# Kernel tuning notes

Hardware: AMD Instinct MI355X
Metric: run time of the kernel (lower is better)

Reference implementation:

```python
import jax, jax.numpy as jnp
import numpy as np

BATCH = 1024
A = 128  # image height
B = 128  # image width (must equal A for the original matmul chain to type-check)
N = 64   # attention grid size
H = 1024 # h_dim


def setup_inputs() -> dict:
    key = jax.random.key(0)
    k0, k1, k2, k3 = jax.random.split(key, 4)
    x = jax.random.normal(k0, (BATCH, A * B), dtype=jnp.float32)
    x_hat = jax.random.normal(k1, (BATCH, A * B), dtype=jnp.float32)
    h = jax.random.normal(k2, (BATCH, H), dtype=jnp.float32)
    W_read_w = jax.random.normal(k3, (5, H), dtype=jnp.float32) * 0.02
    W_read_b = jnp.zeros((5,), dtype=jnp.float32)
    return {"x": x, "x_hat": x_hat, "h": h, "W_read_w": W_read_w, "W_read_b": W_read_b}


def _compute_filterbanks(params):
    # params: (5,) from W_read(h)[0]
    gt_X, gt_Y, log_var, log_dt = params[0], params[1], params[2], params[3]
    var = jnp.exp(log_var + 1e-8)
    # .item() in the original detaches these from the autograd graph
    g_X = jax.lax.stop_gradient((A + 1) * (gt_X + 1) / 2)
    g_Y = jax.lax.stop_gradient((B + 1) * (gt_Y + 1) / 2)
    d = jax.lax.stop_gradient(jnp.exp(log_dt) * (max(A, B) - 1) / (N - 1))
    # linspace(g + (-N/2-0.5)d, g + (N-1-N/2-0.5)d, N) == g + (i - N/2 - 0.5)*d
    idx = jnp.arange(N, dtype=jnp.float32) - N / 2 - 0.5  # (N,)
    mu_X = g_X + idx * d  # (N,)
    mu_Y = g_Y + idx * d  # (N,)
    a = jnp.arange(A, dtype=jnp.float32)
    b = jnp.arange(B, dtype=jnp.float32)
    F_X = jnp.exp(-((a[None, :] - mu_X[:, None]) ** 2) / (2 * var))  # (N, A)
    F_Y = jnp.exp(-((b[None, :] - mu_Y[:, None]) ** 2) / (2 * var))  # (N, B)
    # NOTE: original normalizes by the GLOBAL sum, not per-row
    F_X = F_X / jnp.sum(F_X)
    F_Y = F_Y / jnp.sum(F_Y)
    return F_X, F_Y


def reference(x, x_hat, h, W_read_w, W_read_b):
    # params from FIRST batch element, shared across the whole batch (as in original)
    params = (h @ W_read_w.T + W_read_b)[0]  # (5,)
    gamma = jnp.exp(params[4])
    F_X, F_Y = _compute_filterbanks(params)  # (N,A), (N,B)

    xi = x.reshape(-1, A, B)
    xh = x_hat.reshape(-1, A, B)

    def filt(z):  # gamma * F_Y @ z @ F_X.T  -> (batch, N, N)
        t = jnp.einsum('na,kab->knb', F_Y, z)      # (batch, N, B)
        return gamma * jnp.einsum('knb,mb->knm', t, F_X)

    x_filt = filt(xi).reshape(-1, N * N)
    x_hat_filt = filt(xh).reshape(-1, N * N)
    return jnp.concatenate([x_filt, x_hat_filt], axis=1)  # (batch, 2*N*N)
```

## Files before the change

### kernel.cpp

```cpp
#include <hip/hip_runtime.h>
#include <math.h>

#define AB 128
#define NN 64
#define HD 1024

#define SFZ 256.0f
#define SFF 64.0f
#define DESCALE (1.0f / 1048576.0f)

typedef _Float16 half8 __attribute__((ext_vector_type(8)));
typedef float f32x4 __attribute__((ext_vector_type(4)));
typedef unsigned u32x4 __attribute__((ext_vector_type(4)));


__device__ __forceinline__ float wave_reduce(float v) {
  v += __shfl_down(v, 32);
  v += __shfl_down(v, 16);
  v += __shfl_down(v, 8);
  v += __shfl_down(v, 4);
  v += __shfl_down(v, 2);
  v += __shfl_down(v, 1);
  return v;
}

__global__ __launch_bounds__(1024) void fb_setup(
    const float* __restrict__ h, const float* __restrict__ Ww,
    const float* __restrict__ Wb, void* __restrict__ wsv) {
  __shared__ float redp[16][5];
  __shared__ float reds[16][2];
  __shared__ float sc[5];
  __shared__ float ssum[2];
  const int tid = threadIdx.x;
  const int lane = tid & 63;
  const int wv = tid >> 6;

  const float hv = h[tid];
  float p[5];
#pragma unroll
  for (int j = 0; j < 5; ++j) p[j] = hv * Ww[j * HD + tid];
#pragma unroll
  for (int j = 0; j < 5; ++j) {
    float r = wave_reduce(p[j]);
    if (lane == 0) redp[wv][j] = r;
  }
  __syncthreads();
  if (tid < 5) {
    float s = Wb[tid];
#pragma unroll
    for (int w = 0; w < 16; ++w) s += redp[w][tid];
    sc[tid] = s;
  }
  __syncthreads();

  const float gt_X = sc[0], gt_Y = sc[1], log_var = sc[2], log_dt = sc[3];
  const float var = expf(log_var + 1e-8f);
  const float g_X = (129.0f * (gt_X + 1.0f)) / 2.0f;
  const float g_Y = (129.0f * (gt_Y + 1.0f)) / 2.0f;
  const float d = (expf(log_dt) * 127.0f) / 63.0f;
  const float twovar = 2.0f * var;

  float fyv[8], fxv[8];
  float sY = 0.f, sX = 0.f;
#pragma unroll
  for (int c = 0; c < 8; ++c) {
    const int idx = tid + 1024 * c;
    const int n = idx >> 7;
    const int col = idx & 127;
    const float idxn = (float)n - 32.5f;
    const float muX = g_X + idxn * d;
    const float muY = g_Y + idxn * d;
    const float dx = (float)col - muX;
    const float dy = (float)col - muY;
    const float fx = expf(-(dx * dx) / twovar);
    const float fy = expf(-(dy * dy) / twovar);
    fyv[c] = fy;
    fxv[c] = fx;
    sY += fy;
    sX += fx;
  }
  {
    float rY = wave_reduce(sY);
    float rX = wave_reduce(sX);
    if (lane == 0) { reds[wv][0] = rY; reds[wv][1] = rX; }
  }
  __syncthreads();
  if (tid < 2) {
    float s = 0.f;
#pragma unroll
    for (int w = 0; w < 16; ++w) s += reds[w][tid];
    ssum[tid] = s;
  }
  __syncthreads();
  const float invY = 1.0f / ssum[0];
  const float invX = 1.0f / ssum[1];

  _Float16* FXk = (_Float16*)wsv;
  _Float16* FYhi = (_Float16*)wsv + 2 * NN * AB;
  _Float16* FYlo = FYhi + NN * AB;

#pragma unroll
  for (int c = 0; c < 8; ++c) {
    const int idx = tid + 1024 * c;
    const int n = idx >> 7;
    const int col = idx & 127;
    const float vy = fyv[c] * invY * SFF;
    const float vx = fxv[c] * invX * SFF;
    const _Float16 yh = (_Float16)vy;
    const _Float16 xh2 = (_Float16)vx;
    FYhi[idx] = yh;
    FYlo[idx] = (_Float16)(vy - (float)yh);
    const int kaddr = ((col >> 3) << 9) + (n << 3) + (col & 7);
    FXk[kaddr] = xh2;
    FXk[8192 + kaddr] = (_Float16)(vx - (float)xh2);
  }
  if (tid == 0) ((float*)wsv)[16384] = expf(sc[4]) * DESCALE;
}

__device__ __forceinline__ void split8(const f32x4 z0, const f32x4 z1,
                                       float s, half8& hi, half8& lo) {
#pragma unroll
  for (int e = 0; e < 8; ++e) {
    const float q = (e < 4 ? z0[e] : z1[e - 4]) * s;
    const _Float16 hh = (_Float16)q;
    hi[e] = hh;
    lo[e] = (_Float16)(q - (float)hh);
  }
}

#define ZLD(dst, base, OFF)                                              \
  asm volatile("global_load_dwordx4 %0, %1, off offset:" #OFF            \
               : "=v"(dst) : "v"(base))

#define WAITVM_SB(N)                                                     \
  do {                                                                   \
    asm volatile("s_waitcnt vmcnt(" #N ")");                             \
    __builtin_amdgcn_sched_barrier(0);                                   \
  } while (0)

__global__ __launch_bounds__(256, 4) void fb_filt(
    const float* __restrict__ x, const float* __restrict__ xh,
    const void* __restrict__ wsv, float* __restrict__ out) {
  __shared__ __align__(16) _Float16 S_lds[2 * NN * AB];

  const int tid = threadIdx.x;
  const int lane = tid & 63;
  const int wv = tid >> 6;
  const int l15 = lane & 15;
  const int h4 = lane >> 4;
  const int bid = blockIdx.x;
  const int img = bid >> 1;
  const int which = bid & 1;
  const float* __restrict__ Z = (which ? xh : x) + (size_t)img * (AB * AB);
  const _Float16* __restrict__ FYhi = (const _Float16*)wsv + 2 * NN * AB;
  const _Float16* __restrict__ FYlo = FYhi + NN * AB;
  const float gamma_eff = ((const float*)wsv)[16384];

  {
    const u32x4* __restrict__ src = (const u32x4*)wsv;
    u32x4* __restrict__ dst = (u32x4*)S_lds;
#pragma unroll
    for (int c = 0; c < 8; ++c) dst[c * 256 + tid] = src[c * 256 + tid];
  }
  __syncthreads();

  const float* zb0 = Z + (32 * wv + l15) * AB + 8 * h4;
  const float* zb1 = zb0 + 16 * AB;
  f32x4 z0_0, z0_1, z0_2, z0_3, z1_0, z1_1, z1_2, z1_3;
  f32x4 z2_0, z2_1, z2_2, z2_3, z3_0, z3_1, z3_2, z3_3;
  ZLD(z0_0, zb0, 0);   ZLD(z0_1, zb0, 16);
  ZLD(z0_2, zb1, 0);   ZLD(z0_3, zb1, 16);
  ZLD(z1_0, zb0, 128); ZLD(z1_1, zb0, 144);
  ZLD(z1_2, zb1, 128); ZLD(z1_3, zb1, 144);
  ZLD(z2_0, zb0, 256); ZLD(z2_1, zb0, 272);
  ZLD(z2_2, zb1, 256); ZLD(z2_3, zb1, 272);
  ZLD(z3_0, zb0, 384); ZLD(z3_1, zb0, 400);
  ZLD(z3_2, zb1, 384); ZLD(z3_3, zb1, 400);

  f32x4 acc[4][2];
#pragma unroll
  for (int mt = 0; mt < 4; ++mt)
#pragma unroll
    for (int j = 0; j < 2; ++j) acc[mt][j] = {0.f, 0.f, 0.f, 0.f};

#define S1_KS(KS, WN)                                                          \
  do {                                                                         \
    WAITVM_SB(WN);                                                             \
    half8 bhi0, blo0, bhi1, blo1;                                              \
    split8(z##KS##_0, z##KS##_1, SFZ, bhi0, blo0);                             \
    split8(z##KS##_2, z##KS##_3, SFZ, bhi1, blo1);                             \
    const int gbase = ((4 * (KS) + h4) << 9);                                  \
    _Pragma("unroll")                                                          \
    for (int mt = 0; mt < 4; ++mt) {                                           \
      const _Float16* ap = S_lds + gbase + ((16 * mt + l15) << 3);             \
      const half8 ahi = *(const half8*)ap;                                     \
      const half8 alo = *(const half8*)(ap + 8192);                            \
      acc[mt][0] = __builtin_amdgcn_mfma_f32_16x16x32_f16(ahi, bhi0, acc[mt][0], 0, 0, 0); \
      acc[mt][0] = __builtin_amdgcn_mfma_f32_16x16x32_f16(ahi, blo0, acc[mt][0], 0, 0, 0); \
      acc[mt][0] = __builtin_amdgcn_mfma_f32_16x16x32_f16(alo, bhi0, acc[mt][0], 0, 0, 0); \
      acc[mt][1] = __builtin_amdgcn_mfma_f32_16x16x32_f16(ahi, bhi1, acc[mt][1], 0, 0, 0); \
      acc[mt][1] = __builtin_amdgcn_mfma_f32_16x16x32_f16(ahi, blo1, acc[mt][1], 0, 0, 0); \
      acc[mt][1] = __builtin_amdgcn_mfma_f32_16x16x32_f16(alo, bhi1, acc[mt][1], 0, 0, 0); \
    }                                                                          \
  } while (0)

  S1_KS(0, 12);
  S1_KS(1, 8);
  S1_KS(2, 4);
  S1_KS(3, 0);
#undef S1_KS

  __syncthreads();

  half8 fyh[4], fyl[4];
#pragma unroll
  for (int ks = 0; ks < 4; ++ks) {
    const int foff = (16 * wv + l15) * AB + 32 * ks + 8 * h4;
    fyh[ks] = *(const half8*)(FYhi + foff);
    fyl[ks] = *(const half8*)(FYlo + foff);
  }

#pragma unroll
  for (int mt = 0; mt < 4; ++mt) {
#pragma unroll
    for (int j = 0; j < 2; ++j) {
      const int abase = ((4 * wv + 2 * j + (l15 >> 3)) << 9) + (l15 & 7);
#pragma unroll
      for (int r = 0; r < 4; ++r) {
        const int row = 16 * mt + 4 * h4 + r;
        const float v = acc[mt][j][r];
        const _Float16 hh = (_Float16)v;
        const _Float16 ll = (_Float16)(v - (float)hh);
        S_lds[abase + (row << 3)] = hh;
        S_lds[8192 + abase + (row << 3)] = ll;
      }
    }
  }
  __syncthreads();

  f32x4 acc2[4];
#pragma unroll
  for (int mt = 0; mt < 4; ++mt) acc2[mt] = {0.f, 0.f, 0.f, 0.f};

#pragma unroll
  for (int ks = 0; ks < 4; ++ks) {
    const int gbase = ((4 * ks + h4) << 9);
#pragma unroll
    for (int mt = 0; mt < 4; ++mt) {
      const _Float16* bp = S_lds + gbase + ((16 * mt + l15) << 3);
      const half8 bh = *(const half8*)bp;
      const half8 bl = *(const half8*)(bp + 8192);
      acc2[mt] = __builtin_amdgcn_mfma_f32_16x16x32_f16(fyh[ks], bh, acc2[mt], 0, 0, 0);
      acc2[mt] = __builtin_amdgcn_mfma_f32_16x16x32_f16(fyh[ks], bl, acc2[mt], 0, 0, 0);
      acc2[mt] = __builtin_amdgcn_mfma_f32_16x16x32_f16(fyl[ks], bh, acc2[mt], 0, 0, 0);
    }
  }

  float* __restrict__ ob = out + (size_t)img * 8192 + which * 4096;
#pragma unroll
  for (int mt = 0; mt < 4; ++mt) {
#pragma unroll
    for (int r = 0; r < 4; ++r) {
      ob[(16 * wv + 4 * h4 + r) * 64 + 16 * mt + l15] = acc2[mt][r] * gamma_eff;
    }
  }
}

extern "C" void kernel_launch(void* const* d_in, const int* in_sizes, int n_in,
                              void* d_out, int out_size, void* d_ws, size_t ws_size,
                              hipStream_t stream) {
  const float* x = (const float*)d_in[0];
  const float* xh = (const float*)d_in[1];
  const float* h = (const float*)d_in[2];
  const float* Ww = (const float*)d_in[3];
  const float* Wb = (const float*)d_in[4];
  float* outp = (float*)d_out;

  fb_setup<<<1, 1024, 0, stream>>>(h, Ww, Wb, d_ws);
  fb_filt<<<2048, 256, 0, stream>>>(x, xh, (const void*)d_ws, outp);
}
```

Measured before the change: 178.8 us.

## Assign one image per wave with per-wave LDS staging and pipelined chunk loads

Each wave now processes a whole 128x128 image in four 32-row chunks instead of four waves cooperating on one image. Stage-1 results go to a private LDS region per wave, so the inter-stage __syncthreads barriers disappear. The next chunk's Z and F_Y loads are issued ahead of stage 2 to overlap global memory with MFMA work. F_Y is stored in a K-blocked layout to suit the new loads. The grid shrinks to 512 blocks and occupancy is lowered to 2 blocks per CU because of the larger LDS footprint and register use, which may reduce latency hiding.

Measured after the change: 181.7 us. No clear change (+1.6%).

```diff
diff --git a/kernel.cpp b/kernel.cpp
--- a/kernel.cpp
+++ b/kernel.cpp
@@ -12,6 +12,8 @@
 typedef _Float16 half8 __attribute__((ext_vector_type(8)));
 typedef float f32x4 __attribute__((ext_vector_type(4)));
 typedef unsigned u32x4 __attribute__((ext_vector_type(4)));
+
+#define MFMA16 __builtin_amdgcn_mfma_f32_16x16x32_f16
 
 
 __device__ __forceinline__ float wave_reduce(float v) {
@@ -96,8 +98,7 @@
   const float invX = 1.0f / ssum[1];
 
   _Float16* FXk = (_Float16*)wsv;
-  _Float16* FYhi = (_Float16*)wsv + 2 * NN * AB;
-  _Float16* FYlo = FYhi + NN * AB;
+  _Float16* FYk = (_Float16*)wsv + 2 * NN * AB;
 
 #pragma unroll
   for (int c = 0; c < 8; ++c) {
@@ -108,11 +109,11 @@
     const float vx = fxv[c] * invX * SFF;
     const _Float16 yh = (_Float16)vy;
     const _Float16 xh2 = (_Float16)vx;
-    FYhi[idx] = yh;
-    FYlo[idx] = (_Float16)(vy - (float)yh);
     const int kaddr = ((col >> 3) << 9) + (n << 3) + (col & 7);
     FXk[kaddr] = xh2;
     FXk[8192 + kaddr] = (_Float16)(vx - (float)xh2);
+    FYk[kaddr] = yh;
+    FYk[8192 + kaddr] = (_Float16)(vy - (float)yh);
   }
   if (tid == 0) ((float*)wsv)[16384] = expf(sc[4]) * DESCALE;
 }
@@ -138,23 +139,23 @@
     __builtin_amdgcn_sched_barrier(0);                                   \
   } while (0)
 
-__global__ __launch_bounds__(256, 4) void fb_filt(
+__global__ __launch_bounds__(256, 2) void fb_filt(
     const float* __restrict__ x, const float* __restrict__ xh,
     const void* __restrict__ wsv, float* __restrict__ out) {
-  __shared__ __align__(16) _Float16 S_lds[2 * NN * AB];
+  __shared__ __align__(16) _Float16 S_lds[32768];
 
   const int tid = threadIdx.x;
   const int lane = tid & 63;
   const int wv = tid >> 6;
   const int l15 = lane & 15;
   const int h4 = lane >> 4;
-  const int bid = blockIdx.x;
-  const int img = bid >> 1;
-  const int which = bid & 1;
+  const int slot = (blockIdx.x << 2) | wv;
+  const int img = slot >> 1;
+  const int which = slot & 1;
   const float* __restrict__ Z = (which ? xh : x) + (size_t)img * (AB * AB);
-  const _Float16* __restrict__ FYhi = (const _Float16*)wsv + 2 * NN * AB;
-  const _Float16* __restrict__ FYlo = FYhi + NN * AB;
+  const _Float16* __restrict__ FYk = (const _Float16*)wsv + 2 * NN * AB;
   const float gamma_eff = ((const float*)wsv)[16384];
+  const int Tb = 16384 + (wv << 12);
 
   {
     const u32x4* __restrict__ src = (const u32x4*)wsv;
@@ -164,104 +165,149 @@
   }
   __syncthreads();
 
-  const float* zb0 = Z + (32 * wv + l15) * AB + 8 * h4;
-  const float* zb1 = zb0 + 16 * AB;
   f32x4 z0_0, z0_1, z0_2, z0_3, z1_0, z1_1, z1_2, z1_3;
   f32x4 z2_0, z2_1, z2_2, z2_3, z3_0, z3_1, z3_2, z3_3;
-  ZLD(z0_0, zb0, 0);   ZLD(z0_1, zb0, 16);
-  ZLD(z0_2, zb1, 0);   ZLD(z0_3, zb1, 16);
-  ZLD(z1_0, zb0, 128); ZLD(z1_1, zb0, 144);
-  ZLD(z1_2, zb1, 128); ZLD(z1_3, zb1, 144);
-  ZLD(z2_0, zb0, 256); ZLD(z2_1, zb0, 272);
-  ZLD(z2_2, zb1, 256); ZLD(z2_3, zb1, 272);
-  ZLD(z3_0, zb0, 384); ZLD(z3_1, zb0, 400);
-  ZLD(z3_2, zb1, 384); ZLD(z3_3, zb1, 400);
-
+  half8 fyh[4], fyl[4];
   f32x4 acc[4][2];
-#pragma unroll
-  for (int mt = 0; mt < 4; ++mt)
-#pragma unroll
-    for (int j = 0; j < 2; ++j) acc[mt][j] = {0.f, 0.f, 0.f, 0.f};
-
-#define S1_KS(KS, WN)                                                          \
-  do {                                                                         \
-    WAITVM_SB(WN);                                                             \
-    half8 bhi0, blo0, bhi1, blo1;                                              \
-    split8(z##KS##_0, z##KS##_1, SFZ, bhi0, blo0);                             \
-    split8(z##KS##_2, z##KS##_3, SFZ, bhi1, blo1);                             \
-    const int gbase = ((4 * (KS) + h4) << 9);                                  \
-    _Pragma("unroll")                                                          \
-    for (int mt = 0; mt < 4; ++mt) {                                           \
-      const _Float16* ap = S_lds + gbase + ((16 * mt + l15) << 3);             \
-      const half8 ahi = *(const half8*)ap;                                     \
-      const half8 alo = *(const half8*)(ap + 8192);                            \
-      acc[mt][0] = __builtin_amdgcn_mfma_f32_16x16x32_f16(ahi, bhi0, acc[mt][0], 0, 0, 0); \
-      acc[mt][0] = __builtin_amdgcn_mfma_f32_16x16x32_f16(ahi, blo0, acc[mt][0], 0, 0, 0); \
-      acc[mt][0] = __builtin_amdgcn_mfma_f32_16x16x32_f16(alo, bhi0, acc[mt][0], 0, 0, 0); \
-      acc[mt][1] = __builtin_amdgcn_mfma_f32_16x16x32_f16(ahi, bhi1, acc[mt][1], 0, 0, 0); \
-      acc[mt][1] = __builtin_amdgcn_mfma_f32_16x16x32_f16(ahi, blo1, acc[mt][1], 0, 0, 0); \
-      acc[mt][1] = __builtin_amdgcn_mfma_f32_16x16x32_f16(alo, bhi1, acc[mt][1], 0, 0, 0); \
-    }                                                                          \
-  } while (0)
-
-  S1_KS(0, 12);
-  S1_KS(1, 8);
-  S1_KS(2, 4);
-  S1_KS(3, 0);
-#undef S1_KS
-
-  __syncthreads();
-
-  half8 fyh[4], fyl[4];
-#pragma unroll
-  for (int ks = 0; ks < 4; ++ks) {
-    const int foff = (16 * wv + l15) * AB + 32 * ks + 8 * h4;
-    fyh[ks] = *(const half8*)(FYhi + foff);
-    fyl[ks] = *(const half8*)(FYlo + foff);
-  }
-
-#pragma unroll
-  for (int mt = 0; mt < 4; ++mt) {
-#pragma unroll
-    for (int j = 0; j < 2; ++j) {
-      const int abase = ((4 * wv + 2 * j + (l15 >> 3)) << 9) + (l15 & 7);
+  f32x4 acc2[4][4];
+#pragma unroll
+  for (int nt = 0; nt < 4; ++nt)
+#pragma unroll
+    for (int mt = 0; mt < 4; ++mt) acc2[nt][mt] = {0.f, 0.f, 0.f, 0.f};
+
+#define ISSUE_Z(AC)                                                      \
+  do {                                                                   \
+    const float* zc0_ = Z + (32 * (AC) + l15) * AB + 8 * h4;             \
+    const float* zc1_ = zc0_ + 16 * AB;                                  \
+    ZLD(z0_0, zc0_, 0);   ZLD(z0_1, zc0_, 16);                           \
+    ZLD(z0_2, zc1_, 0);   ZLD(z0_3, zc1_, 16);                           \
+    ZLD(z1_0, zc0_, 128); ZLD(z1_1, zc0_, 144);                          \
+    ZLD(z1_2, zc1_, 128); ZLD(z1_3, zc1_, 144);                          \
+    ZLD(z2_0, zc0_, 256); ZLD(z2_1, zc0_, 272);                          \
+    ZLD(z2_2, zc1_, 256); ZLD(z2_3, zc1_, 272);                          \
+    ZLD(z3_0, zc0_, 384); ZLD(z3_1, zc0_, 400);                          \
+    ZLD(z3_2, zc1_, 384); ZLD(z3_3, zc1_, 400);                          \
+  } while (0)
+
+#define ISSUE_FY(AC)                                                     \
+  do {                                                                   \
+    const _Float16* fh_ = FYk + ((4 * (AC) + h4) << 9) + (l15 << 3);     \
+    const _Float16* fl_ = fh_ + 8192;                                    \
+    ZLD(fyh[0], fh_, 0);   ZLD(fyh[1], fh_, 256);                        \
+    ZLD(fyh[2], fh_, 512); ZLD(fyh[3], fh_, 768);                        \
+    ZLD(fyl[0], fl_, 0);   ZLD(fyl[1], fl_, 256);                        \
+    ZLD(fyl[2], fl_, 512); ZLD(fyl[3], fl_, 768);                        \
+  } while (0)
+
+#define S1(KS, WN)                                                       \
+  do {                                                                   \
+    WAITVM_SB(WN);                                                       \
+    half8 bh0_, bl0_, bh1_, bl1_;                                        \
+    split8(z##KS##_0, z##KS##_1, SFZ, bh0_, bl0_);                       \
+    split8(z##KS##_2, z##KS##_3, SFZ, bh1_, bl1_);                       \
+    const int gb_ = ((4 * (KS) + h4) << 9);                              \
+    _Pragma("unroll")                                                    \
+    for (int mt = 0; mt < 4; ++mt) {                                     \
+      const _Float16* ap_ = S_lds + gb_ + ((16 * mt + l15) << 3);        \
+      const half8 ah_ = *(const half8*)ap_;                              \
+      const half8 al_ = *(const half8*)(ap_ + 8192);                     \
+      acc[mt][0] = MFMA16(ah_, bh0_, acc[mt][0], 0, 0, 0);               \
+      acc[mt][0] = MFMA16(ah_, bl0_, acc[mt][0], 0, 0, 0);               \
+      acc[mt][0] = MFMA16(al_, bh0_, acc[mt][0], 0, 0, 0);               \
+      acc[mt][1] = MFMA16(ah_, bh1_, acc[mt][1], 0, 0, 0);               \
+      acc[mt][1] = MFMA16(ah_, bl1_, acc[mt][1], 0, 0, 0);               \
+      acc[mt][1] = MFMA16(al_, bh1_, acc[mt][1], 0, 0, 0);               \
+    }                                                                    \
+  } while (0)
+
+#define TSTORE                                                           \
+  do {                                                                   \
+    _Pragma("unroll")                                                    \
+    for (int mt = 0; mt < 4; ++mt) {                                     \
+      _Pragma("unroll")                                                  \
+      for (int j = 0; j < 2; ++j) {                                      \
+        const int ab_ = Tb + ((2 * j + (l15 >> 3)) << 9) + (l15 & 7);    \
+        _Pragma("unroll")                                                \
+        for (int r = 0; r < 4; ++r) {                                    \
+          const int row_ = 16 * mt + 4 * h4 + r;                         \
+          const float v_ = acc[mt][j][r];                                \
+          const _Float16 hh_ = (_Float16)v_;                             \
+          const _Float16 ll_ = (_Float16)(v_ - (float)hh_);              \
+          S_lds[ab_ + (row_ << 3)] = hh_;                                \
+          S_lds[ab_ + 2048 + (row_ << 3)] = ll_;                         \
+        }                                                                \
+      }                                                                  \
+    }                                                                    \
+  } while (0)
+
+#define STAGE2                                                           \
+  do {                                                                   \
+    _Pragma("unroll")                                                    \
+    for (int mt = 0; mt < 4; ++mt) {                                     \
+      const _Float16* bp_ = S_lds + Tb + (h4 << 9) + ((16 * mt + l15) << 3); \
+      const half8 bh_ = *(const half8*)bp_;                              \
+      const half8 bl_ = *(const half8*)(bp_ + 2048);                     \
+      _Pragma("unroll")                                                  \
+      for (int nt = 0; nt < 4; ++nt) {                                   \
+        acc2[nt][mt] = MFMA16(fyh[nt], bh_, acc2[nt][mt], 0, 0, 0);      \
+        acc2[nt][mt] = MFMA16(fyh[nt], bl_, acc2[nt][mt], 0, 0, 0);      \
+        acc2[nt][mt] = MFMA16(fyl[nt], bh_, acc2[nt][mt], 0, 0, 0);      \
+      }                                                                  \
+    }                                                                    \
+  } while (0)
+
+#define ZERO_ACC                                                         \
+  do {                                                                   \
+    _Pragma("unroll")                                                    \
+    for (int mt = 0; mt < 4; ++mt) {                                     \
+      acc[mt][0] = {0.f, 0.f, 0.f, 0.f};                                 \
+      acc[mt][1] = {0.f, 0.f, 0.f, 0.f};                                 \
+    }                                                                    \
+  } while (0)
+
+  ISSUE_Z(0);
+  ISSUE_FY(0);
+
+  ZERO_ACC;
+  S1(0, 20); S1(1, 16); S1(2, 12); S1(3, 8);
+  TSTORE;
+  ISSUE_Z(1);
+  WAITVM_SB(16);
+  STAGE2;
+  ISSUE_FY(1);
+
+  ZERO_ACC;
+  S1(0, 20); S1(1, 16); S1(2, 12); S1(3, 8);
+  TSTORE;
+  ISSUE_Z(2);
+  WAITVM_SB(16);
+  STAGE2;
+  ISSUE_FY(2);
+
+  ZERO_ACC;
+  S1(0, 20); S1(1, 16); S1(2, 12); S1(3, 8);
+  TSTORE;
+  ISSUE_Z(3);
+  WAITVM_SB(16);
+  STAGE2;
+  ISSUE_FY(3);
+
+  ZERO_ACC;
+  S1(0, 20); S1(1, 16); S1(2, 12); S1(3, 8);
+  TSTORE;
+  WAITVM_SB(0);
+  STAGE2;
+
+  float* __restrict__ ob = out + (size_t)img * 8192 + which * 4096;
+#pragma unroll
+  for (int nt = 0; nt < 4; ++nt) {
+#pragma unroll
+    for (int mt = 0; mt < 4; ++mt) {
 #pragma unroll
       for (int r = 0; r < 4; ++r) {
-        const int row = 16 * mt + 4 * h4 + r;
-        const float v = acc[mt][j][r];
-        const _Float16 hh = (_Float16)v;
-        const _Float16 ll = (_Float16)(v - (float)hh);
-        S_lds[abase + (row << 3)] = hh;
-        S_lds[8192 + abase + (row << 3)] = ll;
+        ob[(16 * nt + 4 * h4 + r) * 64 + 16 * mt + l15] =
+            acc2[nt][mt][r] * gamma_eff;
       }
-    }
-  }
-  __syncthreads();
-
-  f32x4 acc2[4];
-#pragma unroll
-  for (int mt = 0; mt < 4; ++mt) acc2[mt] = {0.f, 0.f, 0.f, 0.f};
-
-#pragma unroll
-  for (int ks = 0; ks < 4; ++ks) {
-    const int gbase = ((4 * ks + h4) << 9);
-#pragma unroll
-    for (int mt = 0; mt < 4; ++mt) {
-      const _Float16* bp = S_lds + gbase + ((16 * mt + l15) << 3);
-      const half8 bh = *(const half8*)bp;
-      const half8 bl = *(const half8*)(bp + 8192);
-      acc2[mt] = __builtin_amdgcn_mfma_f32_16x16x32_f16(fyh[ks], bh, acc2[mt], 0, 0, 0);
-      acc2[mt] = __builtin_amdgcn_mfma_f32_16x16x32_f16(fyh[ks], bl, acc2[mt], 0, 0, 0);
-      acc2[mt] = __builtin_amdgcn_mfma_f32_16x16x32_f16(fyl[ks], bh, acc2[mt], 0, 0, 0);
-    }
-  }
-
-  float* __restrict__ ob = out + (size_t)img * 8192 + which * 4096;
-#pragma unroll
-  for (int mt = 0; mt < 4; ++mt) {
-#pragma unroll
-    for (int r = 0; r < 4; ++r) {
-      ob[(16 * wv + 4 * h4 + r) * 64 + 16 * mt + l15] = acc2[mt][r] * gamma_eff;
     }
   }
 }
@@ -277,5 +323,5 @@
   float* outp = (float*)d_out;
 
   fb_setup<<<1, 1024, 0, stream>>>(h, Ww, Wb, d_ws);
-  fb_filt<<<2048, 256, 0, stream>>>(x, xh, (const void*)d_ws, outp);
-}
+  fb_filt<<<512, 256, 0, stream>>>(x, xh, (const void*)d_ws, outp);
+}
```
